# Kernel optimization log

Measured on AMD Instinct MI355X. Metric: run time of the kernel, lower is better.

The kernel has to match this reference:

```python
import jax, jax.numpy as jnp
import numpy as np

B, T, J, D = 64, 2048, 128, 256

def setup_inputs() -> dict:
    key = jax.random.key(0)
    k1, k2, k3 = jax.random.split(key, 3)
    H = jax.random.normal(k1, (B, T, D), dtype=jnp.float32)
    U = jax.random.normal(k2, (B, J, D), dtype=jnp.float32)
    w = jax.random.normal(k3, (3 * D, 1), dtype=jnp.float32) * 0.05
    return {"H": H, "U": U, "w": w}


def reference(H, U, w):
    # Original: tile H to (B,T,J,D), tile U to (B,T,J,D), concat [H,U,H*U] -> (B,T,J,3D),
    # then dot with w (3D,1) and squeeze -> (B,T,J).
    # Equivalent trilinear form without materializing the tiled tensor:
    # S[b,t,j] = H[b,t]@w1 + U[b,j]@w2 + (H[b,t]*w3)@U[b,j]
    d = H.shape[-1]
    wv = w[:, 0]
    w1, w2, w3 = wv[:d], wv[d:2 * d], wv[2 * d:]
    s_h = jnp.einsum('btd,d->bt', H, w1)          # (B,T)
    s_u = jnp.einsum('bjd,d->bj', U, w2)          # (B,J)
    s_hu = jnp.einsum('btd,bjd->btj', H * w3, U)  # (B,T,J)
    return s_h[:, :, None] + s_u[:, None, :] + s_hu
```

## Files before the change

kernel.cpp:

```cpp
#include <hip/hip_runtime.h>
#include <stdint.h>

#define Bb 64
#define Tt 2048
#define Jj 128
#define Dd 256


typedef __attribute__((ext_vector_type(8))) __bf16 bf16x8;
typedef __attribute__((ext_vector_type(8))) unsigned short ushort8v;
typedef __attribute__((ext_vector_type(4))) float f32x4;

__device__ __forceinline__ unsigned short f2bf(float f) {
    unsigned int u = __builtin_bit_cast(unsigned int, f);
    u += 0x7FFFu + ((u >> 16) & 1u);
    return (unsigned short)(u >> 16);
}

__device__ __forceinline__ float dot8(const float4& a0, const float4& a1,
                                      const float4& b0, const float4& b1) {
    return a0.x * b0.x + a0.y * b0.y + a0.z * b0.z + a0.w * b0.w +
           a1.x * b1.x + a1.y * b1.y + a1.z * b1.z + a1.w * b1.w;
}

__device__ __forceinline__ bf16x8 pack8(const float4& a0, const float4& a1) {
    ushort8v s;
    s[0] = f2bf(a0.x); s[1] = f2bf(a0.y); s[2] = f2bf(a0.z); s[3] = f2bf(a0.w);
    s[4] = f2bf(a1.x); s[5] = f2bf(a1.y); s[6] = f2bf(a1.z); s[7] = f2bf(a1.w);
    return __builtin_bit_cast(bf16x8, s);
}

__global__ __launch_bounds__(256)
void prep_u(const float* __restrict__ U, const float* __restrict__ w,
            unsigned short* __restrict__ Up) {
    const int idx = blockIdx.x * 256 + threadIdx.x;
    const int b  = idx >> 12;
    const int j  = (idx >> 9) & 7;
    const int ks = (idx >> 6) & 7;
    const int l  = idx & 63;
    const int row = j * 16 + (l & 15);
    const int k0  = ks * 32 + (l >> 4) * 8;

    const float* up = U + ((size_t)(b * Jj + row)) * Dd + k0;
    const float* wp = w + 2 * Dd + k0;
    const float4 u0 = *(const float4*)(up);
    const float4 u1 = *(const float4*)(up + 4);
    const float4 w0 = *(const float4*)(wp);
    const float4 w1 = *(const float4*)(wp + 4);

    ushort8v s;
    s[0] = f2bf(u0.x * w0.x); s[1] = f2bf(u0.y * w0.y);
    s[2] = f2bf(u0.z * w0.z); s[3] = f2bf(u0.w * w0.w);
    s[4] = f2bf(u1.x * w1.x); s[5] = f2bf(u1.y * w1.y);
    s[6] = f2bf(u1.z * w1.z); s[7] = f2bf(u1.w * w1.w);
    ((ushort8v*)Up)[idx] = s;
}

__global__ __launch_bounds__(128)
void prep_su(const float* __restrict__ U, const float* __restrict__ w,
             float* __restrict__ su) {
    const int b = blockIdx.x, col = threadIdx.x;
    const float* up = U + ((size_t)b * Jj + col) * Dd;
    const float* w2 = w + Dd;
    float s = 0.f;
#pragma unroll 4
    for (int d = 0; d < Dd; d += 4) {
        const float4 u = *(const float4*)(up + d);
        const float4 v = *(const float4*)(w2 + d);
        s += u.x * v.x + u.y * v.y + u.z * v.z + u.w * v.w;
    }
    su[b * Jj + col] = s;
}

__global__ __launch_bounds__(256, 4)
void sim_main(const float* __restrict__ H, const unsigned short* __restrict__ Up,
              const float* __restrict__ w, const float* __restrict__ su,
              float* __restrict__ out) {
    const int tid   = threadIdx.x;
    const int wid   = tid >> 6;
    const int lane  = tid & 63;
    const int row16 = lane & 15;
    const int quad  = lane >> 4;

    const int b  = blockIdx.x >> 5;
    const int m0 = ((blockIdx.x & 31) * 4 + wid) * 16;

    const float* Hp = H + ((size_t)(b * Tt + m0 + row16)) * Dd + quad * 8;
    const unsigned short* Ub = Up + (size_t)b * 8 * 8 * 512;
    const float* wq = w + quad * 8;

    f32x4 acc[8];
#pragma unroll
    for (int j = 0; j < 8; ++j) acc[j] = (f32x4){0.f, 0.f, 0.f, 0.f};
    float sh = 0.f;

#pragma unroll 1
    for (int ks = 0; ks < 8; ++ks) {
        const float4 h0 = *(const float4*)(Hp + ks * 32);
        const float4 h1 = *(const float4*)(Hp + ks * 32 + 4);

        bf16x8 bfr[8];
#pragma unroll
        for (int j = 0; j < 8; ++j)
            bfr[j] = __builtin_bit_cast(bf16x8,
                *(const ushort8v*)(Ub + ((size_t)(j * 8 + ks) * 64 + lane) * 8));

        const float4 w1a = *(const float4*)(wq + ks * 32);
        const float4 w1b = *(const float4*)(wq + ks * 32 + 4);
        sh += dot8(h0, h1, w1a, w1b);

        const bf16x8 af = pack8(h0, h1);
#pragma unroll
        for (int j = 0; j < 8; ++j)
            acc[j] = __builtin_amdgcn_mfma_f32_16x16x32_bf16(af, bfr[j], acc[j], 0, 0, 0);
    }

    sh += __shfl_xor(sh, 16);
    sh += __shfl_xor(sh, 32);
    float shv[4];
#pragma unroll
    for (int rg = 0; rg < 4; ++rg)
        shv[rg] = __shfl(sh, quad * 4 + rg);

    float* outW = out + ((size_t)(b * Tt + m0)) * Jj;
    const float* sub = su + b * Jj;
#pragma unroll
    for (int j = 0; j < 8; ++j) {
        const int col = j * 16 + row16;
        const float suv = sub[col];
#pragma unroll
        for (int rg = 0; rg < 4; ++rg)
            outW[(size_t)(quad * 4 + rg) * Jj + col] = acc[j][rg] + shv[rg] + suv;
    }
}

extern "C" void kernel_launch(void* const* d_in, const int* in_sizes, int n_in,
                              void* d_out, int out_size, void* d_ws, size_t ws_size,
                              hipStream_t stream) {
    const float* H = (const float*)d_in[0];
    const float* U = (const float*)d_in[1];
    const float* w = (const float*)d_in[2];
    float* out = (float*)d_out;

    unsigned short* Up = (unsigned short*)d_ws;
    float* su = (float*)((char*)d_ws + (size_t)Bb * Jj * Dd * 2);

    prep_u<<<1024, 256, 0, stream>>>(U, w, Up);
    prep_su<<<Bb, 128, 0, stream>>>(U, w, su);
    sim_main<<<Bb * 32, 256, 0, stream>>>(H, Up, w, su, out);
}
```

Measured before the change: 247.4 us.

## Stage U fragments in LDS, fold w1 dot into MFMA, prefetch H, widen blocks

The main kernel now uses 512-thread blocks that load each batch's packed bf16 U·w3 fragments into shared memory once, so eight waves share them instead of each re-reading from global memory. The H·w1 row term is computed by an extra MFMA against a bf16 w1 column packed by the prep kernel, replacing the scalar FP32 dot and its shuffle reduction. H loads are software-prefetched four k-steps ahead. prep_su becomes a wave-per-row shuffle reduction. Costs are 64KB of LDS per block, which limits occupancy, and the w1 term is now computed in bf16 rather than fp32, which lowers its accuracy.

```diff
diff --git a/kernel.cpp b/kernel.cpp
--- a/kernel.cpp
+++ b/kernel.cpp
@@ -17,12 +17,6 @@
     return (unsigned short)(u >> 16);
 }
 
-__device__ __forceinline__ float dot8(const float4& a0, const float4& a1,
-                                      const float4& b0, const float4& b1) {
-    return a0.x * b0.x + a0.y * b0.y + a0.z * b0.z + a0.w * b0.w +
-           a1.x * b1.x + a1.y * b1.y + a1.z * b1.z + a1.w * b1.w;
-}
-
 __device__ __forceinline__ bf16x8 pack8(const float4& a0, const float4& a1) {
     ushort8v s;
     s[0] = f2bf(a0.x); s[1] = f2bf(a0.y); s[2] = f2bf(a0.z); s[3] = f2bf(a0.w);
@@ -31,96 +25,117 @@
 }
 
 __global__ __launch_bounds__(256)
-void prep_u(const float* __restrict__ U, const float* __restrict__ w,
-            unsigned short* __restrict__ Up) {
+void prep_upw1(const float* __restrict__ U, const float* __restrict__ w,
+               unsigned short* __restrict__ Up) {
     const int idx = blockIdx.x * 256 + threadIdx.x;
-    const int b  = idx >> 12;
-    const int j  = (idx >> 9) & 7;
-    const int ks = (idx >> 6) & 7;
-    const int l  = idx & 63;
-    const int row = j * 16 + (l & 15);
+    const int b   = idx / 4608;
+    const int rem = idx - b * 4608;
+    const int j   = rem >> 9;
+    const int ks  = (rem >> 6) & 7;
+    const int l   = idx & 63;
     const int k0  = ks * 32 + (l >> 4) * 8;
 
-    const float* up = U + ((size_t)(b * Jj + row)) * Dd + k0;
-    const float* wp = w + 2 * Dd + k0;
-    const float4 u0 = *(const float4*)(up);
-    const float4 u1 = *(const float4*)(up + 4);
-    const float4 w0 = *(const float4*)(wp);
-    const float4 w1 = *(const float4*)(wp + 4);
-
     ushort8v s;
-    s[0] = f2bf(u0.x * w0.x); s[1] = f2bf(u0.y * w0.y);
-    s[2] = f2bf(u0.z * w0.z); s[3] = f2bf(u0.w * w0.w);
-    s[4] = f2bf(u1.x * w1.x); s[5] = f2bf(u1.y * w1.y);
-    s[6] = f2bf(u1.z * w1.z); s[7] = f2bf(u1.w * w1.w);
+    if (j < 8) {
+        const int row = j * 16 + (l & 15);
+        const float* up = U + ((size_t)(b * Jj + row)) * Dd + k0;
+        const float* wp = w + 2 * Dd + k0;
+        const float4 u0 = *(const float4*)(up);
+        const float4 u1 = *(const float4*)(up + 4);
+        const float4 w0 = *(const float4*)(wp);
+        const float4 w1 = *(const float4*)(wp + 4);
+        s[0] = f2bf(u0.x * w0.x); s[1] = f2bf(u0.y * w0.y);
+        s[2] = f2bf(u0.z * w0.z); s[3] = f2bf(u0.w * w0.w);
+        s[4] = f2bf(u1.x * w1.x); s[5] = f2bf(u1.y * w1.y);
+        s[6] = f2bf(u1.z * w1.z); s[7] = f2bf(u1.w * w1.w);
+    } else {
+        const bool n0 = (l & 15) == 0;
+#pragma unroll
+        for (int e = 0; e < 8; ++e)
+            s[e] = n0 ? f2bf(w[k0 + e]) : (unsigned short)0;
+    }
     ((ushort8v*)Up)[idx] = s;
 }
 
-__global__ __launch_bounds__(128)
+__global__ __launch_bounds__(256)
 void prep_su(const float* __restrict__ U, const float* __restrict__ w,
              float* __restrict__ su) {
-    const int b = blockIdx.x, col = threadIdx.x;
-    const float* up = U + ((size_t)b * Jj + col) * Dd;
-    const float* w2 = w + Dd;
-    float s = 0.f;
-#pragma unroll 4
-    for (int d = 0; d < Dd; d += 4) {
-        const float4 u = *(const float4*)(up + d);
-        const float4 v = *(const float4*)(w2 + d);
-        s += u.x * v.x + u.y * v.y + u.z * v.z + u.w * v.w;
-    }
-    su[b * Jj + col] = s;
+    const int row  = blockIdx.x * 4 + (threadIdx.x >> 6);
+    const int lane = threadIdx.x & 63;
+    const float4 u = *(const float4*)(U + (size_t)row * Dd + lane * 4);
+    const float4 v = *(const float4*)(w + Dd + lane * 4);
+    float s = u.x * v.x + u.y * v.y + u.z * v.z + u.w * v.w;
+#pragma unroll
+    for (int d = 1; d < 64; d <<= 1) s += __shfl_xor(s, d);
+    if (lane == 0) su[row] = s;
 }
 
-__global__ __launch_bounds__(256, 4)
+__global__ __launch_bounds__(512, 4)
 void sim_main(const float* __restrict__ H, const unsigned short* __restrict__ Up,
-              const float* __restrict__ w, const float* __restrict__ su,
-              float* __restrict__ out) {
+              const float* __restrict__ su, float* __restrict__ out) {
+    __shared__ ushort8v lUp[4096];
+
     const int tid   = threadIdx.x;
     const int wid   = tid >> 6;
     const int lane  = tid & 63;
     const int row16 = lane & 15;
     const int quad  = lane >> 4;
 
-    const int b  = blockIdx.x >> 5;
-    const int m0 = ((blockIdx.x & 31) * 4 + wid) * 16;
+    const int b  = blockIdx.x >> 4;
+    const int m0 = (blockIdx.x & 15) * 128 + wid * 16;
+
+    const ushort8v* Ub = (const ushort8v*)Up + (size_t)b * 9 * 512;
+#pragma unroll
+    for (int p = 0; p < 8; ++p)
+        lUp[tid + p * 512] = Ub[tid + p * 512];
+
+    bf16x8 w1f[8];
+    const ushort8v* Uw1 = Ub + 8 * 512 + lane;
+#pragma unroll
+    for (int ks = 0; ks < 8; ++ks)
+        w1f[ks] = __builtin_bit_cast(bf16x8, Uw1[ks * 64]);
 
     const float* Hp = H + ((size_t)(b * Tt + m0 + row16)) * Dd + quad * 8;
-    const unsigned short* Ub = Up + (size_t)b * 8 * 8 * 512;
-    const float* wq = w + quad * 8;
+    float4 hb0[4], hb1[4];
+#pragma unroll
+    for (int p = 0; p < 4; ++p) {
+        hb0[p] = *(const float4*)(Hp + p * 32);
+        hb1[p] = *(const float4*)(Hp + p * 32 + 4);
+    }
 
     f32x4 acc[8];
 #pragma unroll
     for (int j = 0; j < 8; ++j) acc[j] = (f32x4){0.f, 0.f, 0.f, 0.f};
-    float sh = 0.f;
+    f32x4 accW = (f32x4){0.f, 0.f, 0.f, 0.f};
 
-#pragma unroll 1
+    __syncthreads();
+
+#pragma unroll
     for (int ks = 0; ks < 8; ++ks) {
-        const float4 h0 = *(const float4*)(Hp + ks * 32);
-        const float4 h1 = *(const float4*)(Hp + ks * 32 + 4);
+        const int slot = ks & 3;
+        const float4 h0 = hb0[slot];
+        const float4 h1 = hb1[slot];
+        if (ks < 4) {
+            hb0[slot] = *(const float4*)(Hp + (ks + 4) * 32);
+            hb1[slot] = *(const float4*)(Hp + (ks + 4) * 32 + 4);
+        }
 
         bf16x8 bfr[8];
 #pragma unroll
         for (int j = 0; j < 8; ++j)
-            bfr[j] = __builtin_bit_cast(bf16x8,
-                *(const ushort8v*)(Ub + ((size_t)(j * 8 + ks) * 64 + lane) * 8));
-
-        const float4 w1a = *(const float4*)(wq + ks * 32);
-        const float4 w1b = *(const float4*)(wq + ks * 32 + 4);
-        sh += dot8(h0, h1, w1a, w1b);
+            bfr[j] = __builtin_bit_cast(bf16x8, lUp[(j * 8 + ks) * 64 + lane]);
 
         const bf16x8 af = pack8(h0, h1);
 #pragma unroll
         for (int j = 0; j < 8; ++j)
             acc[j] = __builtin_amdgcn_mfma_f32_16x16x32_bf16(af, bfr[j], acc[j], 0, 0, 0);
+        accW = __builtin_amdgcn_mfma_f32_16x16x32_bf16(af, w1f[ks], accW, 0, 0, 0);
     }
 
-    sh += __shfl_xor(sh, 16);
-    sh += __shfl_xor(sh, 32);
     float shv[4];
 #pragma unroll
     for (int rg = 0; rg < 4; ++rg)
-        shv[rg] = __shfl(sh, quad * 4 + rg);
+        shv[rg] = __shfl(accW[rg], quad * 16);
 
     float* outW = out + ((size_t)(b * Tt + m0)) * Jj;
     const float* sub = su + b * Jj;
@@ -143,9 +158,9 @@
     float* out = (float*)d_out;
 
     unsigned short* Up = (unsigned short*)d_ws;
-    float* su = (float*)((char*)d_ws + (size_t)Bb * Jj * Dd * 2);
+    float* su = (float*)((char*)d_ws + (size_t)Bb * 9 * 512 * 16);
 
-    prep_u<<<1024, 256, 0, stream>>>(U, w, Up);
-    prep_su<<<Bb, 128, 0, stream>>>(U, w, su);
-    sim_main<<<Bb * 32, 256, 0, stream>>>(H, Up, w, su, out);
+    prep_upw1<<<1152, 256, 0, stream>>>(U, w, Up);
+    prep_su<<<Bb * Jj / 4, 256, 0, stream>>>(U, w, su);
+    sim_main<<<Bb * 16, 512, 0, stream>>>(H, Up, su, out);
 }
```

New measurement: 232.7 us. -5.9%, faster.
